# Kernel optimization log

Hardware: AMD Instinct MI355X
Metric: run time of the kernel (lower is better)

The kernel has to match this reference:

```python
import jax, jax.numpy as jnp
import numpy as np

B, H, W, DIM = 16, 28, 28, 256
HEADS, K = 8, 7
HD = DIM // HEADS
MLP = int(DIM * 4.0)
EPS = 1e-5


def setup_inputs() -> dict:
    key = jax.random.key(0)
    ks = jax.random.split(key, 8)
    s = 0.02
    return {
        "x": jax.random.normal(ks[0], (B, H, W, DIM), jnp.float32),
        "norm1_w": jnp.ones((DIM,), jnp.float32),
        "norm1_b": jnp.zeros((DIM,), jnp.float32),
        "qkv_w": jax.random.normal(ks[1], (3 * DIM, DIM), jnp.float32) * s,
        "qkv_b": jnp.zeros((3 * DIM,), jnp.float32),
        "rpb": jax.random.normal(ks[2], (HEADS, 2 * K - 1, 2 * K - 1), jnp.float32) * s,
        "proj_w": jax.random.normal(ks[3], (DIM, DIM), jnp.float32) * s,
        "proj_b": jnp.zeros((DIM,), jnp.float32),
        "norm2_w": jnp.ones((DIM,), jnp.float32),
        "norm2_b": jnp.zeros((DIM,), jnp.float32),
        "fc1_w": jax.random.normal(ks[4], (MLP, DIM), jnp.float32) * s,
        "fc1_b": jnp.zeros((MLP,), jnp.float32),
        "fc2_w": jax.random.normal(ks[5], (DIM, MLP), jnp.float32) * s,
        "fc2_b": jnp.zeros((DIM,), jnp.float32),
    }


def _ln(x, w, b):
    m = jnp.mean(x, axis=-1, keepdims=True)
    v = jnp.var(x, axis=-1, keepdims=True)  # biased, as torch LayerNorm
    return (x - m) * jax.lax.rsqrt(v + EPS) * w + b


def _window_idx(n):
    # NATTEN border handling: window shifts so every query has exactly K neighbors
    start = jnp.clip(jnp.arange(n) - K // 2, 0, n - K)  # [n]
    idx = start[:, None] + jnp.arange(K)                # [n, K] absolute neighbor index
    rel = idx - jnp.arange(n)[:, None] + (K - 1)        # [n, K] rpb index in [0, 2K-2]
    return idx, rel


def _neighborhood_attn(x, qkv_w, qkv_b, rpb, proj_w, proj_b):
    b, h, w, c = x.shape
    qkv = (x @ qkv_w.T + qkv_b).reshape(b, h, w, 3, HEADS, HD)
    q, k, v = qkv[:, :, :, 0], qkv[:, :, :, 1], qkv[:, :, :, 2]  # [b,h,w,heads,hd]
    q = q * (HD ** -0.5)
    idx_h, rel_h = _window_idx(h)
    idx_w, rel_w = _window_idx(w)
    # gather K/V neighborhoods: [b,h,K,w,K,heads,hd]
    kwin = k[:, idx_h][:, :, :, idx_w]
    vwin = v[:, idx_h][:, :, :, idx_w]
    # logits per query (i,j) over its KxK window
    attn = jnp.einsum('bijhd,biajchd->bhijac', q, kwin)  # [b,heads,h,w,K,K]
    bias = rpb[:, rel_h]                 # [heads,h,K,2K-1]
    bias = bias[:, :, :, rel_w]          # [heads,h,K,w,K]
    bias = bias.transpose(0, 1, 3, 2, 4) # [heads,h,w,K,K]
    attn = attn + bias[None]
    attn = jax.nn.softmax(attn.reshape(b, HEADS, h, w, K * K), axis=-1)
    attn = attn.reshape(b, HEADS, h, w, K, K)
    out = jnp.einsum('bhijac,biajchd->bijhd', attn, vwin).reshape(b, h, w, c)
    return out @ proj_w.T + proj_b


def reference(x, norm1_w, norm1_b, qkv_w, qkv_b, rpb, proj_w, proj_b,
              norm2_w, norm2_b, fc1_w, fc1_b, fc2_w, fc2_b):
    shortcut = x
    x = _ln(x, norm1_w, norm1_b)
    x = shortcut + _neighborhood_attn(x, qkv_w, qkv_b, rpb, proj_w, proj_b)
    h = _ln(x, norm2_w, norm2_b) @ fc1_w.T + fc1_b
    h = jax.nn.gelu(h, approximate=False)  # torch nn.GELU default (erf)
    return x + (h @ fc2_w.T + fc2_b)
```

## Files before the change

### kernel.cpp

```cpp
#include <hip/hip_runtime.h>
#include <hip/hip_bf16.h>
#include <math.h>

#define DIM   256
#define HEADS 8
#define HD    32
#define KW    7
#define HH    28
#define WW    28
#define BBATCH 16
#define NTOK  (BBATCH*HH*WW)
#define MLPD  1024
#define EPSLN 1e-5f
#define QSCALE 0.17677669529663687f

#define AS1 __attribute__((address_space(1)))
#define AS3 __attribute__((address_space(3)))

typedef __attribute__((ext_vector_type(8))) short short8;
typedef __attribute__((ext_vector_type(4))) float f32x4;
typedef unsigned short us;

__device__ __forceinline__ float b2f(us u) {
  union { float f; unsigned u; } x; x.u = ((unsigned)u) << 16; return x.f;
}
__device__ __forceinline__ us f2b(float f) {
  union { float f; unsigned u; } x; x.f = f;
  unsigned lsb = (x.u >> 16) & 1;
  x.u += 0x7fffu + lsb;
  return (us)(x.u >> 16);
}
__device__ __forceinline__ bool probe_f32(const us* p) { return p[0] == 0; }

__device__ __forceinline__ void gll16(const us* g, us* l) {
  __builtin_amdgcn_global_load_lds((const AS1 unsigned*)(const void*)g,
                                   (AS3 unsigned*)(void*)l, 16, 0, 0);
}

__device__ __forceinline__ float gelu_f(float x) {
  const float y = 0.7978845608028654f * x * (1.0f + 0.044715f * x * x);
  const float u = __expf(2.0f * y);
  const float th = 1.0f - 2.0f / (u + 1.0f);
  return 0.5f * x * (1.0f + th);
}

__global__ __launch_bounds__(256) void pre_kernel(const void* s0, const void* s1,
                                                  const void* s2, const void* s3,
                                                  us* d0, us* d1, us* d2, us* d3,
                                                  const void* p0, const void* p1, const void* p2,
                                                  const void* p3, const void* p4, const void* p5,
                                                  const void* p6, const void* p7, const void* p8,
                                                  float* __restrict__ pack,
                                                  const void* __restrict__ x,
                                                  us* __restrict__ xn1,
                                                  us* __restrict__ bias_t,
                                                  const us* __restrict__ probe)
{
  const bool isf32 = probe_f32(probe);
  const int blk = blockIdx.x;
  const int t = threadIdx.x;
  if (blk < 768) {
    const int gi = (blk * 256 + t) * 4;
    const void* src; us* dst; int loc; bool qs = false;
    if (gi < 196608)      { src = s0; dst = d0; loc = gi; qs = (loc < 65536); }
    else if (gi < 262144) { src = s1; dst = d1; loc = gi - 196608; }
    else if (gi < 524288) { src = s2; dst = d2; loc = gi - 262144; }
    else                  { src = s3; dst = d3; loc = gi - 524288; }
    float v[4];
    if (isf32) {
      const float4 f = *(const float4*)((const float*)src + loc);
      v[0] = f.x; v[1] = f.y; v[2] = f.z; v[3] = f.w;
    } else {
      ushort4 u = *(const ushort4*)((const us*)src + loc);
      v[0] = b2f(u.x); v[1] = b2f(u.y); v[2] = b2f(u.z); v[3] = b2f(u.w);
    }
    const float sc = qs ? QSCALE : 1.0f;
    ushort4 o;
    o.x = f2b(v[0] * sc); o.y = f2b(v[1] * sc); o.z = f2b(v[2] * sc); o.w = f2b(v[3] * sc);
    *(ushort4*)(dst + loc) = o;
  } else if (blk < 777) {
    const int seg = blk - 768;
    const void* srcs[9] = {p0, p1, p2, p3, p4, p5, p6, p7, p8};
    const int offs[9] = {0, 256, 512, 1280, 1536, 1792, 2048, 3072, 3328};
    const int lens[9] = {256, 256, 768, 256, 256, 256, 1024, 256, 1352};
    const void* s = srcs[seg];
    const int off = offs[seg], len = lens[seg];
    for (int i = t; i < len; i += 256) {
      float v = isf32 ? ((const float*)s)[i] : b2f(((const us*)s)[i]);
      if (seg == 2 && i < 256) v *= QSCALE;
      pack[off + i] = v;
    }
  } else if (blk < 3913) {
    const int wave = t >> 6, lane = t & 63;
    const int tok = (blk - 777) * 4 + wave;
    const int c0 = lane * 4;
    float v[4];
    if (isf32) {
      const float4 f = *(const float4*)((const float*)x + (size_t)tok * DIM + c0);
      v[0] = f.x; v[1] = f.y; v[2] = f.z; v[3] = f.w;
    } else {
      ushort4 u = *(const ushort4*)((const us*)x + (size_t)tok * DIM + c0);
      v[0] = b2f(u.x); v[1] = b2f(u.y); v[2] = b2f(u.z); v[3] = b2f(u.w);
    }
    float s  = v[0] + v[1] + v[2] + v[3];
    float s2 = v[0]*v[0] + v[1]*v[1] + v[2]*v[2] + v[3]*v[3];
    #pragma unroll
    for (int m = 32; m; m >>= 1) { s += __shfl_xor(s, m); s2 += __shfl_xor(s2, m); }
    const float mean = s * (1.0f / DIM);
    const float var  = s2 * (1.0f / DIM) - mean * mean;
    const float rstd = rsqrtf(var + EPSLN);
    float wv[4], bv[4];
    if (isf32) {
      const float4 a = *(const float4*)((const float*)p0 + c0);
      const float4 c = *(const float4*)((const float*)p1 + c0);
      wv[0]=a.x; wv[1]=a.y; wv[2]=a.z; wv[3]=a.w;
      bv[0]=c.x; bv[1]=c.y; bv[2]=c.z; bv[3]=c.w;
    } else {
      ushort4 a = *(const ushort4*)((const us*)p0 + c0);
      ushort4 c = *(const ushort4*)((const us*)p1 + c0);
      wv[0]=b2f(a.x); wv[1]=b2f(a.y); wv[2]=b2f(a.z); wv[3]=b2f(a.w);
      bv[0]=b2f(c.x); bv[1]=b2f(c.y); bv[2]=b2f(c.z); bv[3]=b2f(c.w);
    }
    ushort4 o;
    o.x = f2b((v[0] - mean) * rstd * wv[0] + bv[0]);
    o.y = f2b((v[1] - mean) * rstd * wv[1] + bv[1]);
    o.z = f2b((v[2] - mean) * rstd * wv[2] + bv[2]);
    o.w = f2b((v[3] - mean) * rstd * wv[3] + bv[3]);
    *(ushort4*)(xn1 + (size_t)tok * DIM + c0) = o;
  } else {
    const int ph = blk - 3913;
    const int p  = ph >> 3, h = ph & 7;
    const int i0 = 2 * p;
    const int si0 = min(max(i0 - 3, 0), 21);
    us* bt = bias_t + (size_t)ph * (224 * 64);
    for (int e = 0; e < 56; ++e) {
      const int idx = e * 256 + t;
      const int kv = idx >> 6;
      const int q  = idx & 63;
      const int isub = q >> 5;
      const int cq = q & 31;
      const int iq = i0 + isub;
      const int siq = min(max(iq - 3, 0), 21);
      const int sj  = min(max(cq - 3, 0), 21);
      const int rr  = (kv * 2341) >> 16;
      const int ar  = si0 + rr;
      const int ck  = kv - rr * 28;
      const int dr = ar - siq, dc = ck - sj;
      const bool valid = (cq < 28) && (dr >= 0) && (dr < 7) && (dc >= 0) && (dc < 7);
      float ev = 0.f;
      if (valid) {
        const int ridx = h * 169 + (ar - iq + 6) * 13 + (ck - cq + 6);
        const float bvv = isf32 ? ((const float*)p8)[ridx] : b2f(((const us*)p8)[ridx]);
        ev = __expf(bvv);
      }
      bt[idx] = f2b(ev);
    }
  }
}

__global__ __launch_bounds__(256) void ln_kernel(const us* __restrict__ in,
                                                 const float* __restrict__ w,
                                                 const float* __restrict__ b,
                                                 us* __restrict__ out)
{
  const int t = threadIdx.x;
  const int wave = t >> 6, lane = t & 63;
  const int tok = blockIdx.x * 4 + wave;
  const int c0 = lane * 4;
  ushort4 u = *(const ushort4*)(in + (size_t)tok * DIM + c0);
  float v[4] = {b2f(u.x), b2f(u.y), b2f(u.z), b2f(u.w)};
  float s  = v[0] + v[1] + v[2] + v[3];
  float s2 = v[0]*v[0] + v[1]*v[1] + v[2]*v[2] + v[3]*v[3];
  #pragma unroll
  for (int m = 32; m; m >>= 1) { s += __shfl_xor(s, m); s2 += __shfl_xor(s2, m); }
  const float mean = s * (1.0f / DIM);
  const float var  = s2 * (1.0f / DIM) - mean * mean;
  const float rstd = rsqrtf(var + EPSLN);
  const float4 wv = *(const float4*)(w + c0);
  const float4 bv = *(const float4*)(b + c0);
  ushort4 o;
  o.x = f2b((v[0] - mean) * rstd * wv.x + bv.x);
  o.y = f2b((v[1] - mean) * rstd * wv.y + bv.y);
  o.z = f2b((v[2] - mean) * rstd * wv.z + bv.z);
  o.w = f2b((v[3] - mean) * rstd * wv.w + bv.w);
  *(ushort4*)(out + (size_t)tok * DIM + c0) = o;
}

template<int BM, int BN, int BK, int MODE>
__global__ __launch_bounds__(256) void gemm_kernel(const us* __restrict__ A,
                                                   const us* __restrict__ W,
                                                   const float* __restrict__ bias,
                                                   const void* __restrict__ resid,
                                                   void* __restrict__ out,
                                                   void* __restrict__ out2,
                                                   void* __restrict__ out3,
                                                   int N, int K,
                                                   const us* __restrict__ probe)
{
  constexpr int MF = BM / 32;
  constexpr int NF = BN / 32;
  constexpr int CPR = BK / 8;
  constexpr int ACH = BM * CPR;
  constexpr int BCH = BN * CPR;
  constexpr int ASZ = BM * BK;
  constexpr int BSZ = BN * BK;
  constexpr int TILEB = 2 * (ASZ + BSZ) * 2;
  constexpr int CSB = (MODE == 3) ? BM * BN * 4 : BM * BN * 2;
  constexpr int SMB = TILEB > CSB ? TILEB : CSB;
  __shared__ char smem[SMB];
  us* Asb = (us*)smem;
  us* Bsb = (us*)smem + 2 * ASZ;

  const int t = threadIdx.x;
  const int wave = t >> 6, lane = t & 63;
  const int wm = wave >> 1, wn = wave & 1;
  const int m0 = blockIdx.x * BM;
  const int n0 = blockIdx.y * BN;
  const int lm = lane & 15;
  const int g  = lane >> 4;

  const int NS = K / BK;

  #define STAGE(buf, kk)                                                         \
    {                                                                            \
      _Pragma("unroll")                                                          \
      for (int i = 0; i < ACH / 256; ++i) {                                      \
        const int slot = i * 256 + t;                                            \
        const int gc = slot ^ ((slot >> 3) & 7);                                 \
        gll16(A + (size_t)(m0 + gc / CPR) * K + (kk) + (gc % CPR) * 8,           \
              &Asb[(buf) * ASZ + slot * 8]);                                     \
      }                                                                          \
      _Pragma("unroll")                                                          \
      for (int i = 0; i < BCH / 256; ++i) {                                      \
        const int slot = i * 256 + t;                                            \
        const int gc = slot ^ ((slot >> 3) & 7);                                 \
        gll16(W + (size_t)(n0 + gc / CPR) * K + (kk) + (gc % CPR) * 8,           \
              &Bsb[(buf) * BSZ + slot * 8]);                                     \
      }                                                                          \
    }

  STAGE(0, 0);

  f32x4 acc[MF][NF] = {};
  int cur = 0;
  for (int s = 0; s < NS; ++s) {
    __syncthreads();
    if (s + 1 < NS) STAGE(cur ^ 1, (s + 1) * BK);
    #pragma unroll
    for (int kh = 0; kh < BK / 32; ++kh) {
      short8 a[MF], b[NF];
      #pragma unroll
      for (int mf = 0; mf < MF; ++mf) {
        const int row = wm * (BM / 2) + mf * 16 + lm;
        const int c = row * CPR + kh * 4 + g;
        const int sl = c ^ ((c >> 3) & 7);
        a[mf] = *(const short8*)(const void*)&Asb[cur * ASZ + sl * 8];
      }
      #pragma unroll
      for (int nf = 0; nf < NF; ++nf) {
        const int row = wn * (BN / 2) + nf * 16 + lm;
        const int c = row * CPR + kh * 4 + g;
        const int sl = c ^ ((c >> 3) & 7);
        b[nf] = *(const short8*)(const void*)&Bsb[cur * BSZ + sl * 8];
      }
      #pragma unroll
      for (int mf = 0; mf < MF; ++mf) {
        #pragma unroll
        for (int nf = 0; nf < NF; ++nf)
          acc[mf][nf] = __builtin_amdgcn_mfma_f32_16x16x32_bf16(a[mf], b[nf], acc[mf][nf], 0, 0, 0);
      }
    }
    cur ^= 1;
  }
  #undef STAGE

  const bool isf32 = (MODE == 1 || MODE == 3) ? probe_f32(probe) : false;
  const int col = lm;
  const int rb  = g * 4;
  __syncthreads();

  if (MODE == 0) {
    us* Cs = (us*)smem;
    const bool isV = (n0 >= 512);
    #pragma unroll
    for (int mf = 0; mf < MF; ++mf) {
      #pragma unroll
      for (int nf = 0; nf < NF; ++nf) {
        const int n_loc = wn * (BN / 2) + nf * 16 + col;
        const float bv = bias[n0 + n_loc];
        #pragma unroll
        for (int j = 0; j < 4; ++j) {
          const int m_loc = wm * (BM / 2) + mf * 16 + rb + j;
          const us cv = f2b(acc[mf][nf][j] + bv);
          if (isV) Cs[n_loc * BM + (m_loc ^ ((n_loc & 7) << 3))] = cv;
          else     Cs[m_loc * BN + (n_loc ^ ((m_loc & 7) << 3))] = cv;
        }
      }
    }
    __syncthreads();
    if (!isV) {
      us* dst = (us*)(n0 < 256 ? out : out2);
      const int nc0 = n0 & 255;
      #pragma unroll
      for (int it = 0; it < (BM * BN / 8) / 256; ++it) {
        const int id = it * 256 + t;
        const int m = id >> 4, c = id & 15;
        const uint4 val = *(const uint4*)&Cs[m * BN + (c ^ (m & 7)) * 8];
        *(uint4*)(dst + (size_t)(m0 + m) * 256 + nc0 + c * 8) = val;
      }
    } else {
      us* dst = (us*)out3;
      #pragma unroll
      for (int it = 0; it < (BM * BN / 8) / 256; ++it) {
        const int id = it * 256 + t;
        const int n_loc = id >> 4, mc = id & 15;
        const uint4 val = *(const uint4*)&Cs[n_loc * BM + (mc ^ (n_loc & 7)) * 8];
        *(uint4*)(dst + (size_t)(n0 - 512 + n_loc) * NTOK + m0 + mc * 8) = val;
      }
    }
  } else if (MODE == 3 && isf32) {
    float* Cf = (float*)smem;
    #pragma unroll
    for (int mf = 0; mf < MF; ++mf) {
      #pragma unroll
      for (int nf = 0; nf < NF; ++nf) {
        const int n_loc = wn * (BN / 2) + nf * 16 + col;
        const float bv = bias[n0 + n_loc];
        #pragma unroll
        for (int j = 0; j < 4; ++j) {
          const int m_loc = wm * (BM / 2) + mf * 16 + rb + j;
          const size_t off = (size_t)(m0 + m_loc) * N + (n0 + n_loc);
          float v = acc[mf][nf][j] + bv + b2f(((const us*)resid)[off]);
          Cf[m_loc * BN + (n_loc ^ ((m_loc & 7) << 3))] = v;
        }
      }
    }
    __syncthreads();
    #pragma unroll
    for (int it = 0; it < (BM * BN / 4) / 256; ++it) {
      const int id = it * 256 + t;
      const int m = id / (BN / 4), c = id % (BN / 4);
      const float4 val = *(const float4*)&Cf[m * BN + ((c ^ ((m & 7) << 1)) * 4)];
      *(float4*)((float*)out + (size_t)(m0 + m) * N + n0 + c * 4) = val;
    }
  } else {
    us* Cs = (us*)smem;
    #pragma unroll
    for (int mf = 0; mf < MF; ++mf) {
      #pragma unroll
      for (int nf = 0; nf < NF; ++nf) {
        const int n_loc = wn * (BN / 2) + nf * 16 + col;
        const float bv = bias[n0 + n_loc];
        #pragma unroll
        for (int j = 0; j < 4; ++j) {
          const int m_loc = wm * (BM / 2) + mf * 16 + rb + j;
          const size_t off = (size_t)(m0 + m_loc) * N + (n0 + n_loc);
          float v = acc[mf][nf][j] + bv;
          if (MODE == 1) v += isf32 ? ((const float*)resid)[off] : b2f(((const us*)resid)[off]);
          else if (MODE == 2) v = gelu_f(v);
          else if (MODE == 3) v += b2f(((const us*)resid)[off]);
          Cs[m_loc * BN + (n_loc ^ ((m_loc & 7) << 3))] = f2b(v);
        }
      }
    }
    __syncthreads();
    #pragma unroll
    for (int it = 0; it < (BM * BN / 8) / 256; ++it) {
      const int id = it * 256 + t;
      const int m = id / (BN / 8), c = id % (BN / 8);
      const uint4 val = *(const uint4*)&Cs[m * BN + (c ^ (m & 7)) * 8];
      *(uint4*)((us*)out + (size_t)(m0 + m) * N + n0 + c * 8) = val;
    }
  }
}

__global__ __launch_bounds__(256) void attn_kernel(const us* __restrict__ q_buf,
                                                   const us* __restrict__ kbuf,
                                                   const us* __restrict__ vt,
                                                   const us* __restrict__ bias_t,
                                                   us* __restrict__ out)
{
  __shared__ us KP[64 * 232];
  __shared__ us Vt[32 * 256];

  const int raw = blockIdx.x;
  const int bid = (raw & 7) * 224 + (raw >> 3);
  const int b  = bid & 15;
  const int ph = bid >> 4;
  const int p  = ph >> 3;
  const int h  = ph & 7;
  const int i0 = 2 * p;
  const int t = threadIdx.x;
  const int wave = t >> 6, lane = t & 63;
  const int lm = lane & 15, g = lane >> 4;
  const int kb = g * 8;
  const int si0 = min(max(i0 - 3, 0), 21);

  const us* kgb = kbuf + (size_t)(b * 784 + si0 * 28) * 256 + h * 32;
  #pragma unroll
  for (int p4 = 0; p4 < 3; ++p4) {
    const int s = p4 * 256 + t;
    const int gk = s ^ ((s >> 3) & 7);
    gll16(kgb + (size_t)(gk >> 2) * 256 + (gk & 3) * 8, &KP[s * 8]);
  }
  if (t < 128) {
    const int s = 768 + t;
    const int gk = s ^ ((s >> 3) & 7);
    gll16(kgb + (size_t)(gk >> 2) * 256 + (gk & 3) * 8, &KP[s * 8]);
  }
  const us* vgb = vt + (size_t)(h * 32) * NTOK + b * 784 + si0 * 28;
  #pragma unroll
  for (int p4 = 0; p4 < 4; ++p4) {
    const int s = p4 * 256 + t;
    const int ch = s >> 5;
    const int ck = (s ^ ((s >> 5) & 7)) & 31;
    gll16(vgb + (size_t)ch * NTOK + ck * 8, &Vt[s * 8]);
  }

  const int qcol_l = min((wave & 1) * 16 + lm, 27);
  const int iq = i0 + (wave >> 1);
  const short8 qa = *(const short8*)(const void*)(q_buf + (size_t)(b * 784 + iq * 28 + qcol_l) * 256 + h * 32 + kb);

  __syncthreads();

  f32x4 s[14];
  #pragma unroll
  for (int n = 0; n < 14; ++n) {
    const int c = (n * 16 + lm) * 4 + g;
    const int sl = c ^ ((c >> 3) & 7);
    const short8 kf = *(const short8*)(const void*)&KP[sl * 8];
    f32x4 z = {0.f, 0.f, 0.f, 0.f};
    s[n] = __builtin_amdgcn_mfma_f32_16x16x32_bf16(qa, kf, z, 0, 0, 0);
  }

  __syncthreads();

  const us* bt = bias_t + (size_t)ph * (224 * 64);
  const int qb = wave * 16 + g * 4;
  float acc4[4] = {0.f, 0.f, 0.f, 0.f};
  #pragma unroll
  for (int n = 0; n < 14; ++n) {
    const ushort4 bb = *(const ushort4*)(const void*)&bt[(n * 16 + lm) * 64 + qb];
    const float eb[4] = {b2f(bb.x), b2f(bb.y), b2f(bb.z), b2f(bb.w)};
    #pragma unroll
    for (int jj = 0; jj < 4; ++jj) {
      const float e = __expf(s[n][jj]) * eb[jj];
      acc4[jj] += e;
      KP[(qb + jj) * 232 + n * 16 + lm] = f2b(e);
    }
  }
  float sm[4];
  #pragma unroll
  for (int jj = 0; jj < 4; ++jj) {
    float v = acc4[jj];
    v += __shfl_xor(v, 1); v += __shfl_xor(v, 2);
    v += __shfl_xor(v, 4); v += __shfl_xor(v, 8);
    sm[jj] = v;
  }

  #pragma unroll
  for (int nto = 0; nto < 2; ++nto) {
    f32x4 o = {0.f, 0.f, 0.f, 0.f};
    const int ch = nto * 16 + lm;
    #pragma unroll
    for (int ks = 0; ks < 7; ++ks) {
      const short8 pa = *(const short8*)(const void*)&KP[(wave * 16 + lm) * 232 + ks * 32 + kb];
      const int c = ch * 32 + ks * 4 + g;
      const short8 vb = *(const short8*)(const void*)&Vt[(c ^ (ch & 7)) * 8];
      o = __builtin_amdgcn_mfma_f32_16x16x32_bf16(pa, vb, o, 0, 0, 0);
    }
    #pragma unroll
    for (int jj = 0; jj < 4; ++jj) {
      const int qc = (wave & 1) * 16 + g * 4 + jj;
      if (qc < 28) {
        const float inv = 1.0f / sm[jj];
        out[(size_t)(b * 784 + iq * 28 + qc) * 256 + h * 32 + nto * 16 + lm] = f2b(o[jj] * inv);
      }
    }
  }
}

extern "C" void kernel_launch(void* const* d_in, const int* in_sizes, int n_in,
                              void* d_out, int out_size, void* d_ws, size_t ws_size,
                              hipStream_t stream)
{
  const us* probe = (const us*)d_in[1];

  char* ws = (char*)d_ws;
  us*    wqkv_c = (us*)(ws);
  us*    wproj_c= (us*)(ws + 393216);
  us*    wfc1_c = (us*)(ws + 524288);
  us*    wfc2_c = (us*)(ws + 1048576);
  float* pack   = (float*)(ws + 1572864);
  us*    bias_t = (us*)(ws + 1593344);
  us*    xn1    = (us*)(ws + 4804608);
  us*    q_buf  = (us*)(ws + 11227136);
  us*    k_buf  = (us*)(ws + 17649664);
  us*    vt     = (us*)(ws + 24088576);
  us*    out1   = (us*)(ws + 30527488);
  us*    hbuf   = (us*)(ws + 36950016);
  us*    att    = xn1;
  us*    xn2    = q_buf;

  const float* p_qkvb = pack + 512;
  const float* p_projb= pack + 1280;
  const float* p_n2w  = pack + 1536;
  const float* p_n2b  = pack + 1792;
  const float* p_fc1b = pack + 2048;
  const float* p_fc2b = pack + 3072;

  pre_kernel<<<4025, 256, 0, stream>>>(d_in[3], d_in[6], d_in[10], d_in[12],
                                       wqkv_c, wproj_c, wfc1_c, wfc2_c,
                                       d_in[1], d_in[2], d_in[4], d_in[7], d_in[8], d_in[9],
                                       d_in[11], d_in[13], d_in[5], pack,
                                       d_in[0], xn1, bias_t, probe);
  gemm_kernel<128, 128, 32, 0><<<dim3(NTOK / 128, 768 / 128), 256, 0, stream>>>(
      xn1, wqkv_c, p_qkvb, nullptr, q_buf, k_buf, vt, 768, 256, probe);
  attn_kernel<<<BBATCH * (HH / 2) * HEADS, 256, 0, stream>>>(q_buf, k_buf, vt, bias_t, att);
  gemm_kernel<64, 64, 64, 1><<<dim3(NTOK / 64, DIM / 64), 256, 0, stream>>>(
      att, wproj_c, p_projb, d_in[0], out1, nullptr, nullptr, DIM, 256, probe);
  ln_kernel<<<NTOK / 4, 256, 0, stream>>>(out1, p_n2w, p_n2b, xn2);
  gemm_kernel<128, 128, 32, 2><<<dim3(NTOK / 128, MLPD / 128), 256, 0, stream>>>(
      xn2, wfc1_c, p_fc1b, nullptr, hbuf, nullptr, nullptr, MLPD, 256, probe);
  gemm_kernel<64, 128, 64, 3><<<dim3(NTOK / 64, DIM / 128), 256, 0, stream>>>(
      hbuf, wfc2_c, p_fc2b, out1, d_out, nullptr, nullptr, DIM, MLPD, probe);
}
```

Baseline: 118.7 us.

## Fuse proj GEMM with residual and LayerNorm2; add XCD-aware block swizzle to GEMMs

Adds a dedicated proj kernel that computes a 32x256 row tile per block, adds bias and residual, then computes LayerNorm statistics in-block. It writes both the residual output and the normalized activations, which removes the separate LN kernel launch and one full read of out1. All generic GEMMs switch to a 1-D grid with an XCD-aware swizzle so blocks sharing rows land on the same XCD for L2 reuse. The fused proj uses only 392 blocks with a full-width N tile, which may lower occupancy or parallelism.

```diff
diff --git a/kernel.cpp b/kernel.cpp
--- a/kernel.cpp
+++ b/kernel.cpp
@@ -42,6 +42,12 @@
   const float u = __expf(2.0f * y);
   const float th = 1.0f - 2.0f / (u + 1.0f);
   return 0.5f * x * (1.0f + th);
+}
+
+__device__ __forceinline__ int xcd_swz(int bid, int nb) {
+  const int q = nb >> 3, r = nb & 7;
+  const int xcd = bid & 7, pos = bid >> 3;
+  return (xcd < r ? xcd * (q + 1) : r * (q + 1) + (xcd - r) * q) + pos;
 }
 
 __global__ __launch_bounds__(256) void pre_kernel(const void* s0, const void* s1,
@@ -158,35 +164,7 @@
   }
 }
 
-__global__ __launch_bounds__(256) void ln_kernel(const us* __restrict__ in,
-                                                 const float* __restrict__ w,
-                                                 const float* __restrict__ b,
-                                                 us* __restrict__ out)
-{
-  const int t = threadIdx.x;
-  const int wave = t >> 6, lane = t & 63;
-  const int tok = blockIdx.x * 4 + wave;
-  const int c0 = lane * 4;
-  ushort4 u = *(const ushort4*)(in + (size_t)tok * DIM + c0);
-  float v[4] = {b2f(u.x), b2f(u.y), b2f(u.z), b2f(u.w)};
-  float s  = v[0] + v[1] + v[2] + v[3];
-  float s2 = v[0]*v[0] + v[1]*v[1] + v[2]*v[2] + v[3]*v[3];
-  #pragma unroll
-  for (int m = 32; m; m >>= 1) { s += __shfl_xor(s, m); s2 += __shfl_xor(s2, m); }
-  const float mean = s * (1.0f / DIM);
-  const float var  = s2 * (1.0f / DIM) - mean * mean;
-  const float rstd = rsqrtf(var + EPSLN);
-  const float4 wv = *(const float4*)(w + c0);
-  const float4 bv = *(const float4*)(b + c0);
-  ushort4 o;
-  o.x = f2b((v[0] - mean) * rstd * wv.x + bv.x);
-  o.y = f2b((v[1] - mean) * rstd * wv.y + bv.y);
-  o.z = f2b((v[2] - mean) * rstd * wv.z + bv.z);
-  o.w = f2b((v[3] - mean) * rstd * wv.w + bv.w);
-  *(ushort4*)(out + (size_t)tok * DIM + c0) = o;
-}
-
-template<int BM, int BN, int BK, int MODE>
+template<int BM, int BN, int BK, int NT, int MODE>
 __global__ __launch_bounds__(256) void gemm_kernel(const us* __restrict__ A,
                                                    const us* __restrict__ W,
                                                    const float* __restrict__ bias,
@@ -194,7 +172,7 @@
                                                    void* __restrict__ out,
                                                    void* __restrict__ out2,
                                                    void* __restrict__ out3,
-                                                   int N, int K,
+                                                   int N, int K, int NB,
                                                    const us* __restrict__ probe)
 {
   constexpr int MF = BM / 32;
@@ -214,8 +192,9 @@
   const int t = threadIdx.x;
   const int wave = t >> 6, lane = t & 63;
   const int wm = wave >> 1, wn = wave & 1;
-  const int m0 = blockIdx.x * BM;
-  const int n0 = blockIdx.y * BN;
+  const int sb = xcd_swz(blockIdx.x, NB);
+  const int m0 = (sb / NT) * BM;
+  const int n0 = (sb % NT) * BN;
   const int lm = lane & 15;
   const int g  = lane >> 4;
 
@@ -274,7 +253,7 @@
   }
   #undef STAGE
 
-  const bool isf32 = (MODE == 1 || MODE == 3) ? probe_f32(probe) : false;
+  const bool isf32 = (MODE == 3) ? probe_f32(probe) : false;
   const int col = lm;
   const int rb  = g * 4;
   __syncthreads();
@@ -356,8 +335,7 @@
           const int m_loc = wm * (BM / 2) + mf * 16 + rb + j;
           const size_t off = (size_t)(m0 + m_loc) * N + (n0 + n_loc);
           float v = acc[mf][nf][j] + bv;
-          if (MODE == 1) v += isf32 ? ((const float*)resid)[off] : b2f(((const us*)resid)[off]);
-          else if (MODE == 2) v = gelu_f(v);
+          if (MODE == 2) v = gelu_f(v);
           else if (MODE == 3) v += b2f(((const us*)resid)[off]);
           Cs[m_loc * BN + (n_loc ^ ((m_loc & 7) << 3))] = f2b(v);
         }
@@ -371,6 +349,145 @@
       const uint4 val = *(const uint4*)&Cs[m * BN + (c ^ (m & 7)) * 8];
       *(uint4*)((us*)out + (size_t)(m0 + m) * N + n0 + c * 8) = val;
     }
+  }
+}
+
+__global__ __launch_bounds__(256) void proj_ln_kernel(const us* __restrict__ A,
+                                                      const us* __restrict__ W,
+                                                      const float* __restrict__ bias,
+                                                      const void* __restrict__ resid,
+                                                      const float* __restrict__ w2,
+                                                      const float* __restrict__ b2,
+                                                      us* __restrict__ out1,
+                                                      us* __restrict__ xn2,
+                                                      const us* __restrict__ probe)
+{
+  constexpr int ASZ = 32 * 32;
+  constexpr int BSZ = 256 * 32;
+  __shared__ char smem[2 * (ASZ + BSZ) * 2];
+  __shared__ float st_s[2][32];
+  __shared__ float st_q[2][32];
+  us* Asb = (us*)smem;
+  us* Bsb = (us*)smem + 2 * ASZ;
+
+  const int t = threadIdx.x;
+  const int wave = t >> 6, lane = t & 63;
+  const int wm = wave >> 1, wn = wave & 1;
+  const int sb = (blockIdx.x & 7) * 49 + (blockIdx.x >> 3);
+  const int m0 = sb * 32;
+  const int lm = lane & 15;
+  const int g  = lane >> 4;
+  const bool isf32 = probe_f32(probe);
+
+  #define PSTAGE(buf, kk)                                                        \
+    {                                                                            \
+      if (t < 128) {                                                             \
+        const int gc = t ^ ((t >> 3) & 7);                                       \
+        gll16(A + (size_t)(m0 + (gc >> 2)) * 256 + (kk) + (gc & 3) * 8,          \
+              &Asb[(buf) * ASZ + t * 8]);                                        \
+      }                                                                          \
+      _Pragma("unroll")                                                          \
+      for (int i = 0; i < 4; ++i) {                                              \
+        const int slot = i * 256 + t;                                            \
+        const int gc = slot ^ ((slot >> 3) & 7);                                 \
+        gll16(W + (size_t)(gc >> 2) * 256 + (kk) + (gc & 3) * 8,                 \
+              &Bsb[(buf) * BSZ + slot * 8]);                                     \
+      }                                                                          \
+    }
+
+  PSTAGE(0, 0);
+
+  f32x4 acc[8] = {};
+  int cur = 0;
+  for (int s = 0; s < 8; ++s) {
+    __syncthreads();
+    if (s + 1 < 8) PSTAGE(cur ^ 1, (s + 1) * 32);
+    short8 a;
+    {
+      const int row = wm * 16 + lm;
+      const int c = row * 4 + g;
+      const int sl = c ^ ((c >> 3) & 7);
+      a = *(const short8*)(const void*)&Asb[cur * ASZ + sl * 8];
+    }
+    #pragma unroll
+    for (int nf = 0; nf < 8; ++nf) {
+      const int row = wn * 128 + nf * 16 + lm;
+      const int c = row * 4 + g;
+      const int sl = c ^ ((c >> 3) & 7);
+      const short8 b = *(const short8*)(const void*)&Bsb[cur * BSZ + sl * 8];
+      acc[nf] = __builtin_amdgcn_mfma_f32_16x16x32_bf16(a, b, acc[nf], 0, 0, 0);
+    }
+    cur ^= 1;
+  }
+  #undef PSTAGE
+
+  float ps[4] = {0.f, 0.f, 0.f, 0.f};
+  float pq[4] = {0.f, 0.f, 0.f, 0.f};
+  #pragma unroll
+  for (int nf = 0; nf < 8; ++nf) {
+    const int n_loc = wn * 128 + nf * 16 + lm;
+    const float bv = bias[n_loc];
+    #pragma unroll
+    for (int j = 0; j < 4; ++j) {
+      const int m_loc = wm * 16 + g * 4 + j;
+      const size_t off = (size_t)(m0 + m_loc) * 256 + n_loc;
+      const float rv = isf32 ? ((const float*)resid)[off] : b2f(((const us*)resid)[off]);
+      const float v = acc[nf][j] + bv + rv;
+      acc[nf][j] = v;
+      ps[j] += v; pq[j] += v * v;
+    }
+  }
+  #pragma unroll
+  for (int j = 0; j < 4; ++j) {
+    float s = ps[j], q = pq[j];
+    s += __shfl_xor(s, 1); q += __shfl_xor(q, 1);
+    s += __shfl_xor(s, 2); q += __shfl_xor(q, 2);
+    s += __shfl_xor(s, 4); q += __shfl_xor(q, 4);
+    s += __shfl_xor(s, 8); q += __shfl_xor(q, 8);
+    if (lm == 0) { st_s[wn][wm * 16 + g * 4 + j] = s; st_q[wn][wm * 16 + g * 4 + j] = q; }
+  }
+  __syncthreads();
+
+  float mean[4], rstd[4];
+  #pragma unroll
+  for (int j = 0; j < 4; ++j) {
+    const int row = wm * 16 + g * 4 + j;
+    const float s = st_s[0][row] + st_s[1][row];
+    const float q = st_q[0][row] + st_q[1][row];
+    mean[j] = s * (1.0f / 256.0f);
+    const float var = q * (1.0f / 256.0f) - mean[j] * mean[j];
+    rstd[j] = rsqrtf(var + EPSLN);
+  }
+
+  us* C1 = (us*)smem;
+  us* C2 = (us*)smem + 8192;
+  #pragma unroll
+  for (int nf = 0; nf < 8; ++nf) {
+    const int n_loc = wn * 128 + nf * 16 + lm;
+    const float w2v = w2[n_loc], b2v = b2[n_loc];
+    #pragma unroll
+    for (int j = 0; j < 4; ++j) {
+      const int m_loc = wm * 16 + g * 4 + j;
+      const float v = acc[nf][j];
+      const int sw = n_loc ^ ((m_loc & 7) << 3);
+      C1[m_loc * 256 + sw] = f2b(v);
+      C2[m_loc * 256 + sw] = f2b((v - mean[j]) * rstd[j] * w2v + b2v);
+    }
+  }
+  __syncthreads();
+  #pragma unroll
+  for (int it = 0; it < 4; ++it) {
+    const int id = it * 256 + t;
+    const int m = id >> 5, c = id & 31;
+    const uint4 v1 = *(const uint4*)&C1[m * 256 + (c ^ (m & 7)) * 8];
+    *(uint4*)(out1 + (size_t)(m0 + m) * 256 + c * 8) = v1;
+  }
+  #pragma unroll
+  for (int it = 0; it < 4; ++it) {
+    const int id = it * 256 + t;
+    const int m = id >> 5, c = id & 31;
+    const uint4 v2 = *(const uint4*)&C2[m * 256 + (c ^ (m & 7)) * 8];
+    *(uint4*)(xn2 + (size_t)(m0 + m) * 256 + c * 8) = v2;
   }
 }
 
@@ -514,14 +631,13 @@
                                        d_in[1], d_in[2], d_in[4], d_in[7], d_in[8], d_in[9],
                                        d_in[11], d_in[13], d_in[5], pack,
                                        d_in[0], xn1, bias_t, probe);
-  gemm_kernel<128, 128, 32, 0><<<dim3(NTOK / 128, 768 / 128), 256, 0, stream>>>(
-      xn1, wqkv_c, p_qkvb, nullptr, q_buf, k_buf, vt, 768, 256, probe);
+  gemm_kernel<128, 128, 32, 6, 0><<<588, 256, 0, stream>>>(
+      xn1, wqkv_c, p_qkvb, nullptr, q_buf, k_buf, vt, 768, 256, 588, probe);
   attn_kernel<<<BBATCH * (HH / 2) * HEADS, 256, 0, stream>>>(q_buf, k_buf, vt, bias_t, att);
-  gemm_kernel<64, 64, 64, 1><<<dim3(NTOK / 64, DIM / 64), 256, 0, stream>>>(
-      att, wproj_c, p_projb, d_in[0], out1, nullptr, nullptr, DIM, 256, probe);
-  ln_kernel<<<NTOK / 4, 256, 0, stream>>>(out1, p_n2w, p_n2b, xn2);
-  gemm_kernel<128, 128, 32, 2><<<dim3(NTOK / 128, MLPD / 128), 256, 0, stream>>>(
-      xn2, wfc1_c, p_fc1b, nullptr, hbuf, nullptr, nullptr, MLPD, 256, probe);
-  gemm_kernel<64, 128, 64, 3><<<dim3(NTOK / 64, DIM / 128), 256, 0, stream>>>(
-      hbuf, wfc2_c, p_fc2b, out1, d_out, nullptr, nullptr, DIM, MLPD, probe);
-}
+  proj_ln_kernel<<<392, 256, 0, stream>>>(att, wproj_c, p_projb, d_in[0],
+                                          p_n2w, p_n2b, out1, xn2, probe);
+  gemm_kernel<128, 128, 32, 8, 2><<<784, 256, 0, stream>>>(
+      xn2, wfc1_c, p_fc1b, nullptr, hbuf, nullptr, nullptr, MLPD, 256, 784, probe);
+  gemm_kernel<64, 128, 64, 2, 3><<<392, 256, 0, stream>>>(
+      hbuf, wfc2_c, p_fc2b, out1, d_out, nullptr, nullptr, DIM, MLPD, 392, probe);
+}
```

After: 112.5 us (median of 2 runs). 1.06x faster.
